# Performance work log

Hardware: AMD Instinct MI355X
Metric: run time of the kernel (lower is better)

## Reference

```python
import jax, jax.numpy as jnp
import numpy as np

N_NODES = 2708      # hardcoded in GCN.__init__ (DictLearn(2708, nfeat/2))
NFEAT = 4096
M_DICT = NFEAT // 2 # dictionary atoms
NHID = 1024
NCLASS = 64
POWER_ITER = 100
FISTA_ITER = 20


def power_method(W, key):
    # nm -> largest eigenvalue of W^T W (sigma_max(W)^2)
    X0 = jax.random.normal(key, (1, W.shape[1]), dtype=W.dtype)
    def body(i, carry):
        X, _ = carry
        Xn = (X @ W.T) @ W
        nm = jnp.linalg.norm(Xn)
        return (Xn / nm, nm)
    _, nm = jax.lax.fori_loop(0, POWER_ITER, body, (X0, jnp.float32(1.0)))
    return nm


def soft_threshold(X, lam):
    return jnp.sign(X) * jax.nn.relu(jnp.abs(X) - lam)


def fista(Y, W, lam, key):
    # torch sets W.requires_grad_(False) during sparse coding
    Ws = jax.lax.stop_gradient(W)
    c = power_method(Ws, key)
    eta = 1.0 / c
    Gamma0 = soft_threshold((eta * Ws).T @ Y, lam)   # (m, nfeat)
    Ynorm = jnp.linalg.norm(Y)
    def step(carry, _):
        Gamma, Z, t = carry
        residual = Ws @ Z - Y                         # (n, nfeat)
        Gamma_new = soft_threshold(Z - eta * (Ws.T @ residual), lam / c)
        t_new = (1.0 + jnp.sqrt(1.0 + 4.0 * t * t)) / 2.0
        Z_new = Gamma_new + (t - 1.0) / t_new * (Gamma_new - Gamma)
        nrm = jnp.linalg.norm(residual) / Ynorm
        return (Gamma_new, Z_new, t_new), nrm
    (Gamma, _, _), norms = jax.lax.scan(
        step, (Gamma0, Gamma0, jnp.float32(1.0)), None, length=FISTA_ITER)
    return Gamma, norms


def setup_inputs() -> dict:
    key = jax.random.key(0)
    ks = jax.random.split(key, 7)
    x = jax.random.normal(ks[0], (N_NODES, NFEAT), dtype=jnp.float32)
    # dense stand-in for the normalized sparse adjacency; scaled to keep activations sane
    adj = jax.random.uniform(ks[1], (N_NODES, N_NODES), dtype=jnp.float32) / N_NODES
    stdv1 = 1.0 / np.sqrt(NHID)
    gc1_w = jax.random.uniform(ks[2], (NFEAT, NHID), minval=-stdv1, maxval=stdv1, dtype=jnp.float32)
    gc1_b = jax.random.uniform(ks[3], (NHID,), minval=-stdv1, maxval=stdv1, dtype=jnp.float32)
    stdv2 = 1.0 / np.sqrt(NCLASS)
    gc2_w = jax.random.uniform(ks[4], (NHID, NCLASS), minval=-stdv2, maxval=stdv2, dtype=jnp.float32)
    gc2_b = jax.random.uniform(ks[5], (NCLASS,), minval=-stdv2, maxval=stdv2, dtype=jnp.float32)
    # torch normalizes W in-place via .data, so the learnable leaf IS the normalized dict
    W_dict = jax.random.normal(ks[6], (N_NODES, M_DICT), dtype=jnp.float32)
    W_dict = W_dict / jnp.linalg.norm(W_dict, axis=0, keepdims=True)
    return {"x": x, "adj": adj, "gc1_w": gc1_w, "gc1_b": gc1_b,
            "gc2_w": gc2_w, "gc2_b": gc2_b, "W_dict": W_dict, "K": 1}


def reference(x, adj, gc1_w, gc1_b, gc2_w, gc2_b, W_dict, K):
    # SC='fista' (the only dimensionally consistent path); K acts as lamda
    lam = jnp.float32(K)
    Gamma, norms = fista(x, W_dict, lam, jax.random.key(1))  # (m, nfeat)
    x_dec = W_dict @ Gamma                                   # (n, nfeat)
    h = jax.nn.relu(adj @ (x_dec @ gc1_w) + gc1_b)           # dropout is identity in eval
    out = adj @ (h @ gc2_w) + gc2_b
    return jax.nn.log_softmax(out, axis=1), x_dec, Gamma, norms
```

## Files before the change

kernel.cpp:

```cpp
#include <hip/hip_runtime.h>
#include <cstdint>
#include <cmath>

#define NN_ 2708
#define NF_ 4096
#define MD_ 2048
#define NH_ 1024
#define NC_ 64
#define FITER 20
#define KPAD 2720


typedef _Float16 half8_t __attribute__((ext_vector_type(8)));
typedef _Float16 half4_t __attribute__((ext_vector_type(4)));
typedef float floatx4_t __attribute__((ext_vector_type(4)));

__device__ __forceinline__ float softt(float v, float t) {
    float a = fabsf(v) - t;
    a = a > 0.f ? a : 0.f;
    return copysignf(a, v);
}

__device__ __forceinline__ float blockReduceSum(float v, float* red) {
    int lane = threadIdx.x & 63, wid = threadIdx.x >> 6;
    #pragma unroll
    for (int off = 32; off; off >>= 1) v += __shfl_down(v, off);
    if (lane == 0) red[wid] = v;
    __syncthreads();
    if (wid == 0) {
        int nw = (blockDim.x + 63) >> 6;
        float r = (lane < nw) ? red[lane] : 0.f;
        #pragma unroll
        for (int off = 4; off; off >>= 1) r += __shfl_down(r, off);
        if (lane == 0) red[0] = r;
    }
    __syncthreads();
    float out = red[0];
    __syncthreads();
    return out;
}

__device__ __forceinline__ float erfinv_f(float x) {
    float w = -log1pf(-x * x);
    float p;
    if (w < 5.0f) {
        w -= 2.5f;
        p = 2.81022636e-08f;
        p = fmaf(p, w, 3.43273939e-07f);
        p = fmaf(p, w, -3.5233877e-06f);
        p = fmaf(p, w, -4.39150654e-06f);
        p = fmaf(p, w, 0.00021858087f);
        p = fmaf(p, w, -0.00125372503f);
        p = fmaf(p, w, -0.00417768164f);
        p = fmaf(p, w, 0.246640727f);
        p = fmaf(p, w, 1.50140941f);
    } else {
        w = sqrtf(w) - 3.0f;
        p = -0.000200214257f;
        p = fmaf(p, w, 0.000100950558f);
        p = fmaf(p, w, 0.00134934322f);
        p = fmaf(p, w, -0.00367342844f);
        p = fmaf(p, w, 0.00573950773f);
        p = fmaf(p, w, -0.0076224613f);
        p = fmaf(p, w, 0.00943887047f);
        p = fmaf(p, w, 1.00167406f);
        p = fmaf(p, w, 2.83297682f);
    }
    return p * x;
}

__device__ __forceinline__ float u32_to_normal(uint32_t bits) {
    uint32_t fb = (bits >> 9) | 0x3F800000u;
    float f = __uint_as_float(fb) - 1.0f;
    const float lo = -0.99999994f;
    float u = fmaf(f, 2.0f, lo);
    u = fmaxf(lo, u);
    return 1.41421356f * erfinv_f(u);
}

__global__ void init_x0_kernel(float* __restrict__ X0) {
    int i = blockIdx.x * blockDim.x + threadIdx.x;
    if (i >= MD_ / 2) return;
    uint32_t x0 = (uint32_t)i, x1 = (uint32_t)(i + MD_ / 2);
    const uint32_t k0 = 0u, k1 = 1u, k2 = 0x1BD11BDBu;
    const uint32_t ks[3] = {k0, k1, k2};
    x0 += k0; x1 += k1;
    const int rot[8] = {13, 15, 26, 6, 17, 29, 16, 24};
    #pragma unroll
    for (int g = 0; g < 5; ++g) {
        const int base = (g & 1) ? 4 : 0;
        #pragma unroll
        for (int rr = 0; rr < 4; ++rr) {
            x0 += x1;
            int r = rot[base + rr];
            x1 = (x1 << r) | (x1 >> (32 - r));
            x1 ^= x0;
        }
        x0 += ks[(g + 1) % 3];
        x1 += ks[(g + 2) % 3] + (uint32_t)(g + 1);
    }
    X0[i] = u32_to_normal(x0);
    X0[i + MD_ / 2] = u32_to_normal(x1);
}

__global__ void zero_scal_kernel(float* __restrict__ scal) {
    int t = threadIdx.x;
    if (t < 32) scal[t] = 0.f;
}

__global__ void fill0_kernel(uint32_t* __restrict__ p, int n32) {
    int i = blockIdx.x * blockDim.x + threadIdx.x;
    if (i < n32) p[i] = 0u;
}

__global__ void sumsq_kernel(const float* __restrict__ X, int n, float* __restrict__ acc) {
    __shared__ float red[8];
    float s = 0.f;
    for (size_t i = (size_t)blockIdx.x * blockDim.x + threadIdx.x; i < (size_t)n;
         i += (size_t)gridDim.x * blockDim.x) {
        float v = X[i];
        s += v * v;
    }
    s = blockReduceSum(s, red);
    if (threadIdx.x == 0) atomicAdd(acc, s);
}

__global__ void tsplit_kernel(const float* __restrict__ src, int R, int ld, int Rpad,
                              _Float16* __restrict__ hi, _Float16* __restrict__ lo) {
    __shared__ float t[32][33];
    int rb = blockIdx.y * 32, cb = blockIdx.x * 32;
    int tx = threadIdx.x & 31, ty = threadIdx.x >> 5;
    #pragma unroll
    for (int s = 0; s < 32; s += 8) {
        int r = rb + ty + s, c = cb + tx;
        t[ty + s][tx] = (r < R) ? src[(size_t)r * ld + c] : 0.f;
    }
    __syncthreads();
    #pragma unroll
    for (int s = 0; s < 32; s += 8) {
        int c = cb + ty + s, r = rb + tx;
        float v = t[tx][ty + s];
        _Float16 h = (_Float16)v;
        size_t o = (size_t)c * Rpad + r;
        hi[o] = h;
        lo[o] = (_Float16)(v - (float)h);
    }
}

__global__ void splitrows_hi_kernel(const float* __restrict__ src, int R, int C,
                                    _Float16* __restrict__ hi) {
    int r = blockIdx.x;
    _Float16* d = hi + (size_t)r * C;
    if (r < R) {
        const float* s = src + (size_t)r * C;
        for (int c = threadIdx.x * 4; c < C; c += 1024) {
            float4 v = *reinterpret_cast<const float4*>(s + c);
            half4_t h;
            h[0] = (_Float16)v.x; h[1] = (_Float16)v.y;
            h[2] = (_Float16)v.z; h[3] = (_Float16)v.w;
            *reinterpret_cast<half4_t*>(d + c) = h;
        }
    } else {
        for (int c = threadIdx.x * 4; c < C; c += 1024) {
            half4_t h = {(_Float16)0.f, (_Float16)0.f, (_Float16)0.f, (_Float16)0.f};
            *reinterpret_cast<half4_t*>(d + c) = h;
        }
    }
}

__global__ void splitadj_hi_kernel(const float* __restrict__ adj, _Float16* __restrict__ hi) {
    int r = blockIdx.x;
    bool rok = r < NN_;
    _Float16* d = hi + (size_t)r * KPAD;
    const float* s = adj + (size_t)r * NN_;
    for (int c = threadIdx.x * 4; c < KPAD; c += 1024) {
        half4_t h = {(_Float16)0.f, (_Float16)0.f, (_Float16)0.f, (_Float16)0.f};
        if (rok && c + 3 < NN_) {
            float4 v = *reinterpret_cast<const float4*>(s + c);
            h[0] = (_Float16)v.x; h[1] = (_Float16)v.y;
            h[2] = (_Float16)v.z; h[3] = (_Float16)v.w;
        }
        *reinterpret_cast<half4_t*>(d + c) = h;
    }
}

__global__ void g0_kernel(const float* __restrict__ Bm, const float* __restrict__ scal,
                          float* __restrict__ Gamma,
                          _Float16* __restrict__ Zh, _Float16* __restrict__ Zl) {
    __shared__ float t[32][33];
    int rb = blockIdx.y * 32;
    int cb = blockIdx.x * 32;
    float eta = scal[1], lam = scal[3];
    int tx = threadIdx.x & 31, ty = threadIdx.x >> 5;
    #pragma unroll
    for (int s = 0; s < 32; s += 8) {
        int r = rb + ty + s, c = cb + tx;
        float g = softt(eta * Bm[(size_t)r * NF_ + c], lam);
        Gamma[(size_t)r * NF_ + c] = g;
        t[ty + s][tx] = g;
    }
    __syncthreads();
    #pragma unroll
    for (int s = 0; s < 32; s += 8) {
        int c = cb + ty + s, r = rb + tx;
        float v = t[tx][ty + s];
        _Float16 h = (_Float16)v;
        size_t o = (size_t)c * MD_ + r;
        Zh[o] = h;
        Zl[o] = (_Float16)(v - (float)h);
    }
}

__global__ __launch_bounds__(256)
void papply_kernel(const _Float16* __restrict__ Mh, const _Float16* __restrict__ Ml,
                   const float* __restrict__ Xc, float* __restrict__ Xn, int addI) {
    __shared__ float xs[MD_];
    __shared__ float red[8];
    const int tid = threadIdx.x;
    float ss = 0.f;
    for (int k = tid; k < MD_; k += 256) { float v = Xc[k]; xs[k] = v; ss += v * v; }
    __syncthreads();
    ss = blockReduceSum(ss, red);
    float inv = 1.0f / sqrtf(ss);
    const int w = tid >> 6, l = tid & 63;
    const int r = blockIdx.x * 4 + w;
    const _Float16* mhr = Mh + (size_t)r * MD_;
    const _Float16* mlr = Ml + (size_t)r * MD_;
    float s = 0.f;
    #pragma unroll
    for (int q = 0; q < 8; ++q) {
        int o = (q * 64 + l) * 4;
        half4_t hv = *reinterpret_cast<const half4_t*>(mhr + o);
        half4_t lv = *reinterpret_cast<const half4_t*>(mlr + o);
        float4 xv = *reinterpret_cast<const float4*>(&xs[o]);
        s = fmaf((float)hv[0] + (float)lv[0], xv.x, s);
        s = fmaf((float)hv[1] + (float)lv[1], xv.y, s);
        s = fmaf((float)hv[2] + (float)lv[2], xv.z, s);
        s = fmaf((float)hv[3] + (float)lv[3], xv.w, s);
    }
    #pragma unroll
    for (int off = 32; off; off >>= 1) s += __shfl_down(s, off);
    if (l == 0) Xn[r] = (s + (addI ? xs[r] : 0.f)) * inv;
}

__global__ void pfinal_kernel(const float* __restrict__ Xf, const int* __restrict__ Kp,
                              float* __restrict__ scal) {
    __shared__ float red[8];
    float ss = 0.f;
    for (int k = threadIdx.x; k < MD_; k += 256) { float v = Xf[k]; ss += v * v; }
    ss = blockReduceSum(ss, red);
    if (threadIdx.x == 0) {
        float c = sqrtf(ss);
        float lam = (float)Kp[0];
        scal[0] = c;
        scal[1] = 1.0f / c;
        scal[2] = lam / c;
        scal[3] = lam;
    }
}

enum { ME_STORE = 0, ME_SYMSPLIT = 1, ME_SYMSPLIT_MI = 2, ME_H1 = 3, ME_SYMSPLIT16 = 4,
       ME_SPLIT_T = 5, ME_FISTAG = 6, ME_FISTAG_LAST = 7, ME_BIAS = 8, ME_BIASRELU = 9 };

__device__ __forceinline__ void stage_h(const _Float16* __restrict__ g, int row0, int K, int kk,
                                        _Float16* s, int tid) {
    const int row = tid >> 2;
    const int kg = (tid & 3) ^ ((row >> 1) & 3);
    const _Float16* gp = g + (size_t)(row0 + row) * K + kk + (kg << 3);
    _Float16* lp = s + ((size_t)((tid >> 6) * 64) << 3);
    __builtin_amdgcn_global_load_lds(
        (const __attribute__((address_space(1))) void*)gp,
        (__attribute__((address_space(3))) void*)lp, 16, 0, 0);
}

template <bool AFP32, bool THREE>
__global__ __launch_bounds__(512)
void mgemm_kernel(const _Float16* __restrict__ Ah, const _Float16* __restrict__ Al,
                  const float* __restrict__ Afp, int Marr,
                  const _Float16* __restrict__ Bh, const _Float16* __restrict__ Bl,
                  int K, int Mvalid, int Nvalid, int ldc,
                  float* __restrict__ C, const float* __restrict__ BmP,
                  const float* __restrict__ bias,
                  _Float16* __restrict__ Th, _Float16* __restrict__ Tl, int Tstride,
                  const float* __restrict__ scal, float betak,
                  float* __restrict__ nrm_acc, int epi) {
    constexpr int TILE = 128 * 32;
    constexpr int NT = AFP32 ? 4 : (THREE ? 8 : 6);
    __shared__ __align__(16) _Float16 smem[NT * TILE];
    float* red = (float*)smem;
    const int tid = threadIdx.x;
    const int w = tid >> 6, l = tid & 63;
    const int wr = w >> 2, wc = w & 3;
    const int quad = l >> 4, lc = l & 15;
    const int row0 = blockIdx.y * 128, col0 = blockIdx.x * 128;
    const int qs = (quad ^ ((lc >> 1) & 3)) << 3;

    floatx4_t acc[4][2];
    #pragma unroll
    for (int i = 0; i < 4; ++i)
        #pragma unroll
        for (int j = 0; j < 2; ++j) {
            floatx4_t z = {0.f, 0.f, 0.f, 0.f};
            acc[i][j] = z;
        }

    if constexpr (!AFP32) {
        _Float16* bAh = smem;
        _Float16* bAl = smem + 2 * TILE;
        _Float16* bBh = smem + (THREE ? 4 : 2) * TILE;
        _Float16* bBl = smem + (THREE ? 6 : 4) * TILE;
        stage_h(Ah, row0, K, 0, bAh, tid);
        if constexpr (THREE) stage_h(Al, row0, K, 0, bAl, tid);
        stage_h(Bh, col0, K, 0, bBh, tid);
        stage_h(Bl, col0, K, 0, bBl, tid);
        asm volatile("s_waitcnt vmcnt(0)" ::: "memory");
        __syncthreads();
        for (int kk = 0; kk < K; kk += 32) {
            const int cur = (kk >> 5) & 1, nxt = cur ^ 1;
            if (kk + 32 < K) {
                stage_h(Ah, row0, K, kk + 32, bAh + nxt * TILE, tid);
                if constexpr (THREE) stage_h(Al, row0, K, kk + 32, bAl + nxt * TILE, tid);
                stage_h(Bh, col0, K, kk + 32, bBh + nxt * TILE, tid);
                stage_h(Bl, col0, K, kk + 32, bBl + nxt * TILE, tid);
            }
            const _Float16* pAh = bAh + cur * TILE;
            const _Float16* pAl = bAl + cur * TILE;
            const _Float16* pBh = bBh + cur * TILE;
            const _Float16* pBl = bBl + cur * TILE;
            half8_t fAh[4], fAl[4], fBh[2], fBl[2];
            #pragma unroll
            for (int i = 0; i < 4; ++i) {
                int oa = (wr * 64 + i * 16 + lc) * 32 + qs;
                fAh[i] = *reinterpret_cast<const half8_t*>(&pAh[oa]);
                if constexpr (THREE) fAl[i] = *reinterpret_cast<const half8_t*>(&pAl[oa]);
            }
            #pragma unroll
            for (int j = 0; j < 2; ++j) {
                int ob = (wc * 32 + j * 16 + lc) * 32 + qs;
                fBh[j] = *reinterpret_cast<const half8_t*>(&pBh[ob]);
                fBl[j] = *reinterpret_cast<const half8_t*>(&pBl[ob]);
            }
            #pragma unroll
            for (int i = 0; i < 4; ++i)
                #pragma unroll
                for (int j = 0; j < 2; ++j) {
                    acc[i][j] = __builtin_amdgcn_mfma_f32_16x16x32_f16(fAh[i], fBh[j], acc[i][j], 0, 0, 0);
                    acc[i][j] = __builtin_amdgcn_mfma_f32_16x16x32_f16(fAh[i], fBl[j], acc[i][j], 0, 0, 0);
                    if constexpr (THREE)
                        acc[i][j] = __builtin_amdgcn_mfma_f32_16x16x32_f16(fAl[i], fBh[j], acc[i][j], 0, 0, 0);
                }
            asm volatile("s_waitcnt vmcnt(0)" ::: "memory");
            __syncthreads();
        }
    } else {
        _Float16* sAh = smem;
        _Float16* sAl = smem + TILE;
        _Float16* sBh = smem + 2 * TILE;
        _Float16* sBl = smem + 3 * TILE;
        for (int kk = 0; kk < K; kk += 32) {
            #pragma unroll
            for (int p = 0; p < 2; ++p) {
                int c2 = p * 512 + tid;
                int r = c2 >> 3, k4 = (c2 & 7) << 2;
                int gr = row0 + r;
                gr = gr < Marr ? gr : Marr - 1;
                float4 v = *reinterpret_cast<const float4*>(Afp + (size_t)gr * K + kk + k4);
                half4_t hh, ll;
                hh[0] = (_Float16)v.x; ll[0] = (_Float16)(v.x - (float)hh[0]);
                hh[1] = (_Float16)v.y; ll[1] = (_Float16)(v.y - (float)hh[1]);
                hh[2] = (_Float16)v.z; ll[2] = (_Float16)(v.z - (float)hh[2]);
                hh[3] = (_Float16)v.w; ll[3] = (_Float16)(v.w - (float)hh[3]);
                int sw = (((k4 >> 3) ^ ((r >> 1) & 3)) << 3) | (k4 & 7);
                *reinterpret_cast<half4_t*>(&sAh[r * 32 + sw]) = hh;
                *reinterpret_cast<half4_t*>(&sAl[r * 32 + sw]) = ll;
            }
            stage_h(Bh, col0, K, kk, sBh, tid);
            stage_h(Bl, col0, K, kk, sBl, tid);
            asm volatile("s_waitcnt vmcnt(0)" ::: "memory");
            __syncthreads();

            half8_t fAh[4], fAl[4], fBh[2], fBl[2];
            #pragma unroll
            for (int i = 0; i < 4; ++i) {
                int oa = (wr * 64 + i * 16 + lc) * 32 + qs;
                fAh[i] = *reinterpret_cast<const half8_t*>(&sAh[oa]);
                fAl[i] = *reinterpret_cast<const half8_t*>(&sAl[oa]);
            }
            #pragma unroll
            for (int j = 0; j < 2; ++j) {
                int ob = (wc * 32 + j * 16 + lc) * 32 + qs;
                fBh[j] = *reinterpret_cast<const half8_t*>(&sBh[ob]);
                fBl[j] = *reinterpret_cast<const half8_t*>(&sBl[ob]);
            }
            #pragma unroll
            for (int i = 0; i < 4; ++i)
                #pragma unroll
                for (int j = 0; j < 2; ++j) {
                    acc[i][j] = __builtin_amdgcn_mfma_f32_16x16x32_f16(fAh[i], fBh[j], acc[i][j], 0, 0, 0);
                    acc[i][j] = __builtin_amdgcn_mfma_f32_16x16x32_f16(fAh[i], fBl[j], acc[i][j], 0, 0, 0);
                    acc[i][j] = __builtin_amdgcn_mfma_f32_16x16x32_f16(fAl[i], fBh[j], acc[i][j], 0, 0, 0);
                }
            __syncthreads();
        }
    }

    float eta = 0.f, thr = 0.f;
    if (epi == ME_FISTAG || epi == ME_FISTAG_LAST) { eta = scal[1]; thr = scal[2]; }
    float rsq = 0.f;
    #pragma unroll
    for (int i = 0; i < 4; ++i) {
        int grow0 = row0 + wr * 64 + i * 16 + quad * 4;
        bool rowok = grow0 < Mvalid;
        #pragma unroll
        for (int j = 0; j < 2; ++j) {
            int gcol = col0 + wc * 32 + j * 16 + lc;
            bool colok = gcol < Nvalid;
            floatx4_t v = acc[i][j];
            if (epi == ME_STORE) {
                if (rowok && colok) {
                    #pragma unroll
                    for (int r = 0; r < 4; ++r) C[(size_t)(grow0 + r) * ldc + gcol] = v[r];
                }
            } else if (epi == ME_SYMSPLIT || epi == ME_SYMSPLIT_MI || epi == ME_H1 ||
                       epi == ME_SYMSPLIT16) {
                #pragma unroll
                for (int r = 0; r < 4; ++r) {
                    float vv = v[r];
                    float dg = ((grow0 + r) == gcol) ? 1.f : 0.f;
                    size_t o = (size_t)(grow0 + r) * Tstride + gcol;
                    if (epi == ME_SYMSPLIT_MI) {
                        vv -= dg;
                    } else if (epi == ME_H1) {
                        float ev = (float)Ah[o] + (float)Al[o];
                        vv = (vv + 2.f * ev + dg) * 0.0625f;
                    } else if (epi == ME_SYMSPLIT16) {
                        vv *= 16.f;
                    }
                    _Float16 h = (_Float16)vv;
                    Th[o] = h;
                    Tl[o] = (_Float16)(vv - (float)h);
                }
            } else if (epi == ME_SPLIT_T) {
                if (rowok && colok) {
                    half4_t hh, ll;
                    #pragma unroll
                    for (int r = 0; r < 4; ++r) {
                        _Float16 h = (_Float16)v[r];
                        hh[r] = h; ll[r] = (_Float16)(v[r] - (float)h);
                    }
                    size_t to = (size_t)gcol * Tstride + grow0;
                    *reinterpret_cast<half4_t*>(&Th[to]) = hh;
                    *reinterpret_cast<half4_t*>(&Tl[to]) = ll;
                }
            } else if (epi == ME_FISTAG || epi == ME_FISTAG_LAST) {
                size_t to = (size_t)gcol * Tstride + grow0;
                half4_t zh = *reinterpret_cast<const half4_t*>(&Bh[to]);
                half4_t zl = *reinterpret_cast<const half4_t*>(&Bl[to]);
                half4_t oh, ol;
                #pragma unroll
                for (int r = 0; r < 4; ++r) {
                    float z = (float)zh[r] + (float)zl[r];
                    float p = v[r] + z;
                    float bi = BmP[(size_t)(grow0 + r) * NF_ + gcol];
                    rsq = fmaf(z, p - 2.0f * bi, rsq);
                    float g = z - eta * (p - bi);
                    float gn = softt(g, thr);
                    size_t ci = (size_t)(grow0 + r) * NF_ + gcol;
                    float gold = C[ci];
                    C[ci] = gn;
                    float zo = (epi == ME_FISTAG) ? (gn + betak * (gn - gold)) : gn;
                    _Float16 h = (_Float16)zo;
                    oh[r] = h; ol[r] = (_Float16)(zo - (float)h);
                }
                *reinterpret_cast<half4_t*>(&Th[to]) = oh;
                *reinterpret_cast<half4_t*>(&Tl[to]) = ol;
            } else {
                if (rowok && colok) {
                    #pragma unroll
                    for (int r = 0; r < 4; ++r) {
                        float s = v[r] + bias[gcol];
                        if (epi == ME_BIASRELU) s = s > 0.f ? s : 0.f;
                        C[(size_t)(grow0 + r) * ldc + gcol] = s;
                    }
                }
            }
        }
    }
    if (epi == ME_FISTAG || epi == ME_FISTAG_LAST) {
        float tot = blockReduceSum(rsq, red);
        if (tid == 0) atomicAdd(nrm_acc, tot);
    }
}

__global__ void logsoftmax_kernel(const float* __restrict__ O, float* __restrict__ out) {
    int row = blockIdx.x * 4 + (threadIdx.x >> 6);
    int lane = threadIdx.x & 63;
    if (row >= NN_) return;
    float v = O[row * NC_ + lane];
    float m = v;
    #pragma unroll
    for (int off = 32; off; off >>= 1) m = fmaxf(m, __shfl_xor(m, off));
    float e = expf(v - m);
    float s = e;
    #pragma unroll
    for (int off = 32; off; off >>= 1) s += __shfl_xor(s, off);
    out[row * NC_ + lane] = (v - m) - logf(s);
}

__global__ void norms_kernel(const float* __restrict__ scal, float* __restrict__ nout) {
    int k = threadIdx.x;
    if (k < FITER) {
        float ysq = scal[4];
        float v = scal[5 + k] + ysq;
        nout[k] = sqrtf(fmaxf(v, 0.f)) / sqrtf(ysq);
    }
}

static inline void launch_m(bool afp32, bool three, dim3 grid,
                            const _Float16* Ah, const _Float16* Al,
                            const float* Afp, int Marr,
                            const _Float16* Bh, const _Float16* Bl,
                            int K, int Mvalid, int Nvalid, int ldc,
                            float* C, const float* BmP, const float* bias,
                            _Float16* Th, _Float16* Tl, int Tstride,
                            const float* scal, float betak, float* nrm, int epi,
                            hipStream_t s) {
    if (afp32)
        mgemm_kernel<true, true><<<grid, dim3(512), 0, s>>>(
            Ah, Al, Afp, Marr, Bh, Bl, K, Mvalid, Nvalid, ldc, C, BmP, bias,
            Th, Tl, Tstride, scal, betak, nrm, epi);
    else if (three)
        mgemm_kernel<false, true><<<grid, dim3(512), 0, s>>>(
            Ah, Al, Afp, Marr, Bh, Bl, K, Mvalid, Nvalid, ldc, C, BmP, bias,
            Th, Tl, Tstride, scal, betak, nrm, epi);
    else
        mgemm_kernel<false, false><<<grid, dim3(512), 0, s>>>(
            Ah, Al, Afp, Marr, Bh, Bl, K, Mvalid, Nvalid, ldc, C, BmP, bias,
            Th, Tl, Tstride, scal, betak, nrm, epi);
}

extern "C" void kernel_launch(void* const* d_in, const int* in_sizes, int n_in,
                              void* d_out, int out_size, void* d_ws, size_t ws_size,
                              hipStream_t stream) {
    const float* x     = (const float*)d_in[0];
    const float* adj   = (const float*)d_in[1];
    const float* gc1_w = (const float*)d_in[2];
    const float* gc1_b = (const float*)d_in[3];
    const float* gc2_w = (const float*)d_in[4];
    const float* gc2_b = (const float*)d_in[5];
    const float* Wd    = (const float*)d_in[6];
    const int*   Kp    = (const int*)d_in[7];

    float* out = (float*)d_out;
    float* logp    = out;
    float* x_dec   = logp + (size_t)NN_ * NC_;
    float* Gamma   = x_dec + (size_t)NN_ * NF_;
    float* norms_o = Gamma + (size_t)MD_ * NF_;

    char* wsb = (char*)d_ws;
    const size_t OFF_R1 = 16512;
    const size_t OFF_R2 = OFF_R1 + 16777216;
    const size_t OFF_R3 = OFF_R2 + 33554432;
    const size_t OFF_R4 = OFF_R3 + 33554432;
    float* scal = (float*)wsb;
    float* Xa   = scal + 32;
    float* Xb   = Xa + MD_;
    _Float16* Eh = (_Float16*)(wsb + OFF_R1);
    _Float16* El = Eh + (size_t)MD_ * MD_;
    float* Bm = (float*)(wsb + OFF_R2);
    _Float16* Wt_hi  = (_Float16*)(wsb + OFF_R3);
    _Float16* Wt_lo  = Wt_hi + (size_t)MD_ * KPAD;
    _Float16* xth_hi = Wt_lo + (size_t)MD_ * KPAD;
    _Float16* xth_lo = (_Float16*)(wsb + OFF_R4);
    _Float16* HA_hi = (_Float16*)(wsb + OFF_R4);
    _Float16* HA_lo = HA_hi + (size_t)MD_ * MD_;
    _Float16* HB_hi = (_Float16*)(wsb + OFF_R3);
    _Float16* HB_lo = HB_hi + (size_t)MD_ * MD_;
    _Float16* ZA_hi = (_Float16*)(wsb + OFF_R3);
    _Float16* ZA_lo = ZA_hi + (size_t)NF_ * MD_;
    _Float16* ZB_hi = (_Float16*)x_dec;
    _Float16* ZB_lo = ZB_hi + (size_t)NF_ * MD_;
    _Float16* adjT_hi = (_Float16*)(wsb + OFF_R2);
    _Float16* xwT_hi  = (_Float16*)(wsb + OFF_R2 + 15319040);
    _Float16* xwT_lo  = xwT_hi + (size_t)NH_ * KPAD;
    _Float16* g1t_hi  = (_Float16*)(wsb + OFF_R1);
    _Float16* g1t_lo  = g1t_hi + (size_t)NH_ * NF_;
    _Float16* xdh     = (_Float16*)(wsb + OFF_R3);
    float*    hbuf    = (float*)(wsb + OFF_R3);
    _Float16* Wh      = (_Float16*)(wsb + OFF_R4);
    _Float16* g2t_hi  = (_Float16*)(wsb + OFF_R4 + 11534336);
    _Float16* g2t_lo  = g2t_hi + (size_t)128 * NH_;
    _Float16* hwT_hi  = (_Float16*)(wsb + OFF_R4 + 12058624);
    _Float16* hwT_lo  = hwT_hi + (size_t)128 * KPAD;
    float*    obuf    = (float*)(wsb + OFF_R4 + 13451264);

    const _Float16* nullh = nullptr;
    float* nullf = nullptr;

    zero_scal_kernel<<<1, 64, 0, stream>>>(scal);
    init_x0_kernel<<<4, 256, 0, stream>>>(Xa);
    sumsq_kernel<<<1024, 256, 0, stream>>>(x, NN_ * NF_, scal + 4);

    tsplit_kernel<<<dim3(MD_ / 32, KPAD / 32), 256, 0, stream>>>(Wd, NN_, MD_, KPAD, Wt_hi, Wt_lo);
    launch_m(false, true, dim3(16, 16), Wt_hi, Wt_lo, nullptr, 0, Wt_hi, Wt_lo,
             KPAD, MD_, MD_, 0, nullf, nullptr, nullptr, Eh, El, MD_,
             scal, 0.f, nullptr, ME_SYMSPLIT_MI, stream);
    for (int half = 0; half < 2; ++half) {
        tsplit_kernel<<<dim3(MD_ / 32, KPAD / 32), 256, 0, stream>>>(
            x + half * 2048, NN_, NF_, KPAD, xth_hi, xth_lo);
        launch_m(false, false, dim3(16, 16), Wt_hi, Wt_lo, nullptr, 0, xth_hi, xth_lo,
                 KPAD, MD_, MD_, NF_, Bm + half * 2048, nullptr, nullptr,
                 nullptr, nullptr, 0, scal, 0.f, nullptr, ME_STORE, stream);
    }
    launch_m(false, false, dim3(16, 16), Eh, El, nullptr, 0, Eh, El,
             MD_, MD_, MD_, 0, nullf, nullptr, nullptr, HA_hi, HA_lo, MD_,
             scal, 0.f, nullptr, ME_H1, stream);
    launch_m(false, false, dim3(16, 16), HA_hi, HA_lo, nullptr, 0, HA_hi, HA_lo,
             MD_, MD_, MD_, 0, nullf, nullptr, nullptr, HB_hi, HB_lo, MD_,
             scal, 0.f, nullptr, ME_SYMSPLIT, stream);
    launch_m(false, false, dim3(16, 16), HB_hi, HB_lo, nullptr, 0, HB_hi, HB_lo,
             MD_, MD_, MD_, 0, nullf, nullptr, nullptr, HA_hi, HA_lo, MD_,
             scal, 0.f, nullptr, ME_SYMSPLIT, stream);
    launch_m(false, false, dim3(16, 16), HA_hi, HA_lo, nullptr, 0, HA_hi, HA_lo,
             MD_, MD_, MD_, 0, nullf, nullptr, nullptr, HB_hi, HB_lo, MD_,
             scal, 0.f, nullptr, ME_SYMSPLIT, stream);
    launch_m(false, false, dim3(16, 16), HB_hi, HB_lo, nullptr, 0, HB_hi, HB_lo,
             MD_, MD_, MD_, 0, nullf, nullptr, nullptr, HA_hi, HA_lo, MD_,
             scal, 0.f, nullptr, ME_SYMSPLIT16, stream);
    for (int it = 0; it < 7; ++it) {
        const _Float16* mh = (it < 3) ? HA_hi : Eh;
        const _Float16* ml = (it < 3) ? HA_lo : El;
        const float* xin = (it & 1) ? Xb : Xa;
        float* xout = (it & 1) ? Xa : Xb;
        papply_kernel<<<MD_ / 4, 256, 0, stream>>>(mh, ml, xin, xout, (it >= 3) ? 1 : 0);
    }
    pfinal_kernel<<<1, 256, 0, stream>>>(Xb, Kp, scal);
    g0_kernel<<<dim3(NF_ / 32, MD_ / 32), 256, 0, stream>>>(Bm, scal, Gamma, ZA_hi, ZA_lo);

    {
        float t = 1.f;
        for (int k = 0; k < FITER; ++k) {
            float tn = (1.0f + sqrtf(1.0f + (4.0f * t) * t)) / 2.0f;
            float beta = (t - 1.0f) / tn;
            t = tn;
            _Float16* in_hi  = (k & 1) ? ZB_hi : ZA_hi;
            _Float16* in_lo  = (k & 1) ? ZB_lo : ZA_lo;
            _Float16* out_hi = (k & 1) ? ZA_hi : ZB_hi;
            _Float16* out_lo = (k & 1) ? ZA_lo : ZB_lo;
            launch_m(false, false, dim3(32, 16), Eh, El, nullptr, 0, in_hi, in_lo,
                     MD_, MD_, NF_, NF_, Gamma, Bm, nullptr,
                     out_hi, out_lo, MD_, scal, beta, scal + 5 + k,
                     (k == FITER - 1) ? ME_FISTAG_LAST : ME_FISTAG, stream);
        }
    }

    splitadj_hi_kernel<<<2816, 256, 0, stream>>>(adj, adjT_hi);
    splitrows_hi_kernel<<<2816, 256, 0, stream>>>(Wd, NN_, MD_, Wh);
    launch_m(false, false, dim3(32, 22), Wh, Wh, nullptr, 0, ZA_hi, ZA_lo,
             MD_, NN_, NF_, NF_, x_dec, nullptr, nullptr,
             nullptr, nullptr, 0, scal, 0.f, nullptr, ME_STORE, stream);
    splitrows_hi_kernel<<<2816, 256, 0, stream>>>(x_dec, NN_, NF_, xdh);
    tsplit_kernel<<<dim3(NH_ / 32, NF_ / 32), 256, 0, stream>>>(gc1_w, NF_, NH_, NF_, g1t_hi, g1t_lo);
    fill0_kernel<<<(2785280 + 255) / 256, 256, 0, stream>>>((uint32_t*)xwT_hi, 2785280);
    launch_m(false, false, dim3(8, 22), xdh, xdh, nullptr, 0, g1t_hi, g1t_lo,
             NF_, NN_, NH_, 0, nullf, nullptr, nullptr,
             xwT_hi, xwT_lo, KPAD, scal, 0.f, nullptr, ME_SPLIT_T, stream);
    launch_m(false, false, dim3(8, 22), adjT_hi, adjT_hi, nullptr, 0, xwT_hi, xwT_lo,
             KPAD, NN_, NH_, NH_, hbuf, nullptr, gc1_b,
             nullptr, nullptr, 0, scal, 0.f, nullptr, ME_BIASRELU, stream);
    fill0_kernel<<<(131072 + 255) / 256, 256, 0, stream>>>((uint32_t*)g2t_hi, 131072);
    tsplit_kernel<<<dim3(NC_ / 32, NH_ / 32), 256, 0, stream>>>(gc2_w, NH_, NC_, NH_, g2t_hi, g2t_lo);
    fill0_kernel<<<(348160 + 255) / 256, 256, 0, stream>>>((uint32_t*)hwT_hi, 348160);
    launch_m(true, true, dim3(1, 22), nullh, nullh, hbuf, NN_, g2t_hi, g2t_lo,
             NH_, NN_, NC_, 0, nullf, nullptr, nullptr,
             hwT_hi, hwT_lo, KPAD, scal, 0.f, nullptr, ME_SPLIT_T, stream);
    launch_m(false, false, dim3(1, 22), adjT_hi, adjT_hi, nullptr, 0, hwT_hi, hwT_lo,
             KPAD, NN_, NC_, NC_, obuf, nullptr, gc2_b,
             nullptr, nullptr, 0, scal, 0.f, nullptr, ME_BIAS, stream);
    logsoftmax_kernel<<<(NN_ + 3) / 4, 256, 0, stream>>>(obuf, logp);
    norms_kernel<<<1, 32, 0, stream>>>(scal, norms_o);
}
```

Baseline: 3.145 ms.

## Triple-buffer fp16 GEMM K-loop and remap workgroups across XCDs

The half-precision GEMM main loop changes from double buffering to a three-stage LDS ring. Loads for tile t+2 are issued while tile t is computed, and partial vmcnt waits let one stage stay in flight across each barrier. Workgroup IDs are also remapped so that consecutive logical tiles land on the same XCD, which should improve L2 reuse of shared A/B panels. The cost is more LDS per block (12 or 9 tiles instead of 8 or 6), which may lower occupancy; loop-variable renames accompany the new `r` used in the remap.

```diff
diff --git a/kernel.cpp b/kernel.cpp
--- a/kernel.cpp
+++ b/kernel.cpp
@@ -285,14 +285,22 @@
                   const float* __restrict__ scal, float betak,
                   float* __restrict__ nrm_acc, int epi) {
     constexpr int TILE = 128 * 32;
-    constexpr int NT = AFP32 ? 4 : (THREE ? 8 : 6);
+    constexpr int TPB = THREE ? 4 : 3;
+    constexpr int NT = AFP32 ? 4 : 3 * TPB;
     __shared__ __align__(16) _Float16 smem[NT * TILE];
     float* red = (float*)smem;
     const int tid = threadIdx.x;
     const int w = tid >> 6, l = tid & 63;
     const int wr = w >> 2, wc = w & 3;
     const int quad = l >> 4, lc = l & 15;
-    const int row0 = blockIdx.y * 128, col0 = blockIdx.x * 128;
+
+    const int nwg = gridDim.x * gridDim.y;
+    const int orig = blockIdx.y * gridDim.x + blockIdx.x;
+    const int xcd = orig & 7, idx = orig >> 3;
+    const int q = nwg >> 3, r = nwg & 7;
+    const int wgid = (xcd < r ? xcd * (q + 1) : r * (q + 1) + (xcd - r) * q) + idx;
+    const int row0 = (wgid / gridDim.x) * 128, col0 = (wgid % gridDim.x) * 128;
+
     const int qs = (quad ^ ((lc >> 1) & 3)) << 3;
 
     floatx4_t acc[4][2];
@@ -305,28 +313,31 @@
         }
 
     if constexpr (!AFP32) {
-        _Float16* bAh = smem;
-        _Float16* bAl = smem + 2 * TILE;
-        _Float16* bBh = smem + (THREE ? 4 : 2) * TILE;
-        _Float16* bBl = smem + (THREE ? 6 : 4) * TILE;
-        stage_h(Ah, row0, K, 0, bAh, tid);
-        if constexpr (THREE) stage_h(Al, row0, K, 0, bAl, tid);
-        stage_h(Bh, col0, K, 0, bBh, tid);
-        stage_h(Bl, col0, K, 0, bBl, tid);
-        asm volatile("s_waitcnt vmcnt(0)" ::: "memory");
-        __syncthreads();
-        for (int kk = 0; kk < K; kk += 32) {
-            const int cur = (kk >> 5) & 1, nxt = cur ^ 1;
-            if (kk + 32 < K) {
-                stage_h(Ah, row0, K, kk + 32, bAh + nxt * TILE, tid);
-                if constexpr (THREE) stage_h(Al, row0, K, kk + 32, bAl + nxt * TILE, tid);
-                stage_h(Bh, col0, K, kk + 32, bBh + nxt * TILE, tid);
-                stage_h(Bl, col0, K, kk + 32, bBl + nxt * TILE, tid);
-            }
-            const _Float16* pAh = bAh + cur * TILE;
-            const _Float16* pAl = bAl + cur * TILE;
-            const _Float16* pBh = bBh + cur * TILE;
-            const _Float16* pBl = bBl + cur * TILE;
+        const int NTK = K >> 5;
+        auto STAGE = [&](int kt, int b) {
+            _Float16* base = smem + b * (TPB * TILE);
+            stage_h(Ah, row0, K, kt << 5, base, tid);
+            if constexpr (THREE) stage_h(Al, row0, K, kt << 5, base + TILE, tid);
+            stage_h(Bh, col0, K, kt << 5, base + (THREE ? 2 : 1) * TILE, tid);
+            stage_h(Bl, col0, K, kt << 5, base + (THREE ? 3 : 2) * TILE, tid);
+        };
+        STAGE(0, 0);
+        if (NTK > 1) {
+            STAGE(1, 1);
+            if constexpr (THREE) asm volatile("s_waitcnt vmcnt(4)" ::: "memory");
+            else                 asm volatile("s_waitcnt vmcnt(3)" ::: "memory");
+        } else {
+            asm volatile("s_waitcnt vmcnt(0)" ::: "memory");
+        }
+        __builtin_amdgcn_s_barrier();
+        for (int t = 0; t < NTK; ++t) {
+            const int cur = t % 3;
+            if (t + 2 < NTK) STAGE(t + 2, (t + 2) % 3);
+            const _Float16* base = smem + cur * (TPB * TILE);
+            const _Float16* pAh = base;
+            const _Float16* pAl = base + TILE;
+            const _Float16* pBh = base + (THREE ? 2 : 1) * TILE;
+            const _Float16* pBl = base + (THREE ? 3 : 2) * TILE;
             half8_t fAh[4], fAl[4], fBh[2], fBl[2];
             #pragma unroll
             for (int i = 0; i < 4; ++i) {
@@ -349,8 +360,14 @@
                     if constexpr (THREE)
                         acc[i][j] = __builtin_amdgcn_mfma_f32_16x16x32_f16(fAl[i], fBh[j], acc[i][j], 0, 0, 0);
                 }
-            asm volatile("s_waitcnt vmcnt(0)" ::: "memory");
-            __syncthreads();
+            __builtin_amdgcn_sched_barrier(0);
+            if (t + 2 < NTK) {
+                if constexpr (THREE) asm volatile("s_waitcnt vmcnt(4)" ::: "memory");
+                else                 asm volatile("s_waitcnt vmcnt(3)" ::: "memory");
+            } else {
+                asm volatile("s_waitcnt vmcnt(0)" ::: "memory");
+            }
+            __builtin_amdgcn_s_barrier();
         }
     } else {
         _Float16* sAh = smem;
@@ -361,8 +378,8 @@
             #pragma unroll
             for (int p = 0; p < 2; ++p) {
                 int c2 = p * 512 + tid;
-                int r = c2 >> 3, k4 = (c2 & 7) << 2;
-                int gr = row0 + r;
+                int r2 = c2 >> 3, k4 = (c2 & 7) << 2;
+                int gr = row0 + r2;
                 gr = gr < Marr ? gr : Marr - 1;
                 float4 v = *reinterpret_cast<const float4*>(Afp + (size_t)gr * K + kk + k4);
                 half4_t hh, ll;
@@ -370,9 +387,9 @@
                 hh[1] = (_Float16)v.y; ll[1] = (_Float16)(v.y - (float)hh[1]);
                 hh[2] = (_Float16)v.z; ll[2] = (_Float16)(v.z - (float)hh[2]);
                 hh[3] = (_Float16)v.w; ll[3] = (_Float16)(v.w - (float)hh[3]);
-                int sw = (((k4 >> 3) ^ ((r >> 1) & 3)) << 3) | (k4 & 7);
-                *reinterpret_cast<half4_t*>(&sAh[r * 32 + sw]) = hh;
-                *reinterpret_cast<half4_t*>(&sAl[r * 32 + sw]) = ll;
+                int sw = (((k4 >> 3) ^ ((r2 >> 1) & 3)) << 3) | (k4 & 7);
+                *reinterpret_cast<half4_t*>(&sAh[r2 * 32 + sw]) = hh;
+                *reinterpret_cast<half4_t*>(&sAl[r2 * 32 + sw]) = ll;
             }
             stage_h(Bh, col0, K, kk, sBh, tid);
             stage_h(Bl, col0, K, kk, sBl, tid);
@@ -419,15 +436,15 @@
             if (epi == ME_STORE) {
                 if (rowok && colok) {
                     #pragma unroll
-                    for (int r = 0; r < 4; ++r) C[(size_t)(grow0 + r) * ldc + gcol] = v[r];
+                    for (int r2 = 0; r2 < 4; ++r2) C[(size_t)(grow0 + r2) * ldc + gcol] = v[r2];
                 }
             } else if (epi == ME_SYMSPLIT || epi == ME_SYMSPLIT_MI || epi == ME_H1 ||
                        epi == ME_SYMSPLIT16) {
                 #pragma unroll
-                for (int r = 0; r < 4; ++r) {
-                    float vv = v[r];
-                    float dg = ((grow0 + r) == gcol) ? 1.f : 0.f;
-                    size_t o = (size_t)(grow0 + r) * Tstride + gcol;
+                for (int r2 = 0; r2 < 4; ++r2) {
+                    float vv = v[r2];
+                    float dg = ((grow0 + r2) == gcol) ? 1.f : 0.f;
+                    size_t o = (size_t)(grow0 + r2) * Tstride + gcol;
                     if (epi == ME_SYMSPLIT_MI) {
                         vv -= dg;
                     } else if (epi == ME_H1) {
@@ -444,9 +461,9 @@
                 if (rowok && colok) {
                     half4_t hh, ll;
                     #pragma unroll
-                    for (int r = 0; r < 4; ++r) {
-                        _Float16 h = (_Float16)v[r];
-                        hh[r] = h; ll[r] = (_Float16)(v[r] - (float)h);
+                    for (int r2 = 0; r2 < 4; ++r2) {
+                        _Float16 h = (_Float16)v[r2];
+                        hh[r2] = h; ll[r2] = (_Float16)(v[r2] - (float)h);
                     }
                     size_t to = (size_t)gcol * Tstride + grow0;
                     *reinterpret_cast<half4_t*>(&Th[to]) = hh;
@@ -458,29 +475,29 @@
                 half4_t zl = *reinterpret_cast<const half4_t*>(&Bl[to]);
                 half4_t oh, ol;
                 #pragma unroll
-                for (int r = 0; r < 4; ++r) {
-                    float z = (float)zh[r] + (float)zl[r];
-                    float p = v[r] + z;
-                    float bi = BmP[(size_t)(grow0 + r) * NF_ + gcol];
+                for (int r2 = 0; r2 < 4; ++r2) {
+                    float z = (float)zh[r2] + (float)zl[r2];
+                    float p = v[r2] + z;
+                    float bi = BmP[(size_t)(grow0 + r2) * NF_ + gcol];
                     rsq = fmaf(z, p - 2.0f * bi, rsq);
                     float g = z - eta * (p - bi);
                     float gn = softt(g, thr);
-                    size_t ci = (size_t)(grow0 + r) * NF_ + gcol;
+                    size_t ci = (size_t)(grow0 + r2) * NF_ + gcol;
                     float gold = C[ci];
                     C[ci] = gn;
                     float zo = (epi == ME_FISTAG) ? (gn + betak * (gn - gold)) : gn;
                     _Float16 h = (_Float16)zo;
-                    oh[r] = h; ol[r] = (_Float16)(zo - (float)h);
+                    oh[r2] = h; ol[r2] = (_Float16)(zo - (float)h);
                 }
                 *reinterpret_cast<half4_t*>(&Th[to]) = oh;
                 *reinterpret_cast<half4_t*>(&Tl[to]) = ol;
             } else {
                 if (rowok && colok) {
                     #pragma unroll
-                    for (int r = 0; r < 4; ++r) {
-                        float s = v[r] + bias[gcol];
+                    for (int r2 = 0; r2 < 4; ++r2) {
+                        float s = v[r2] + bias[gcol];
                         if (epi == ME_BIASRELU) s = s > 0.f ? s : 0.f;
-                        C[(size_t)(grow0 + r) * ldc + gcol] = s;
+                        C[(size_t)(grow0 + r2) * ldc + gcol] = s;
                     }
                 }
             }
```

Measured after the change: 3.303 ms. 5.0% more time.
